# Optimization experiments

Hardware: AMD Instinct MI355X
Metric: run time of the kernel (lower is better)

## Reference

```python
import jax, jax.numpy as jnp
import numpy as np

N_NODES = 100000


def gat_conv(x, edge_index, W, att_src, att_dst, bias, concat=True, negative_slope=0.2):
    """PyG-style GATConv (eval mode, dropout off, self-loops added)."""
    N = x.shape[0]
    H, C = att_src.shape
    # add self loops (PyG default add_self_loops=True)
    ar = jnp.arange(N, dtype=edge_index.dtype)
    ei = jnp.concatenate([edge_index, jnp.stack([ar, ar])], axis=1)
    src, dst = ei[0], ei[1]

    h = (x @ W).reshape(N, H, C)                       # [N,H,C]
    a_src = (h * att_src[None]).sum(-1)                # [N,H]
    a_dst = (h * att_dst[None]).sum(-1)                # [N,H]

    e = jax.nn.leaky_relu(a_src[src] + a_dst[dst], negative_slope)  # [E,H]
    # segment softmax over destination nodes
    e_max = jax.ops.segment_max(e, dst, num_segments=N)            # [N,H]
    ex = jnp.exp(e - jax.lax.stop_gradient(e_max)[dst])
    denom = jax.ops.segment_sum(ex, dst, num_segments=N)           # [N,H]
    alpha = ex / (denom[dst] + 1e-16)                              # [E,H]

    out = jax.ops.segment_sum(alpha[:, :, None] * h[src], dst, num_segments=N)  # [N,H,C]
    out = out.reshape(N, H * C) if concat else out.mean(axis=1)
    return out + bias


def setup_inputs() -> dict:
    key = jax.random.key(0)
    ks = jax.random.split(key, 9)
    N, E, F_in, H, C = N_NODES, 3200000, 16, 4, 8
    x = jax.random.normal(ks[0], (N, F_in), dtype=jnp.float32)
    edge_index = jax.random.randint(ks[1], (2, E), 0, N, dtype=jnp.int64)
    s1 = 1.0 / np.sqrt(F_in)
    s2 = 1.0 / np.sqrt(H * C)
    return {
        "x": x,
        "edge_index": edge_index,
        "W1": jax.random.normal(ks[2], (F_in, H * C), dtype=jnp.float32) * s1,
        "att_src1": jax.random.normal(ks[3], (H, C), dtype=jnp.float32) * s2,
        "att_dst1": jax.random.normal(ks[4], (H, C), dtype=jnp.float32) * s2,
        "b1": jnp.zeros((H * C,), dtype=jnp.float32),
        "W2": jax.random.normal(ks[5], (H * C, 1), dtype=jnp.float32) * s2,
        "att_src2": jax.random.normal(ks[6], (1, 1), dtype=jnp.float32),
        "att_dst2": jax.random.normal(ks[7], (1, 1), dtype=jnp.float32),
        "b2": jnp.zeros((1,), dtype=jnp.float32),
    }


def reference(x, edge_index, W1, att_src1, att_dst1, b1, W2, att_src2, att_dst2, b2):
    h = jax.nn.elu(gat_conv(x, edge_index, W1, att_src1, att_dst1, b1, concat=True))
    return gat_conv(h, edge_index, W2, att_src2, att_dst2, b2, concat=False)
```

## Files before the change

### kernel.cpp

```cpp
#include <hip/hip_runtime.h>

#define LRELU_SLOPE 0.2f
#define BN 64
#define BSH 6
#define NC 2048
#define CAP 3840
#define TILE 16384

__device__ __forceinline__ float lrelu(float x) { return x > 0.f ? x : LRELU_SLOPE * x; }
__device__ __forceinline__ float eexp(float x)  { return __expf(fminf(x, 80.f)); }

__device__ __forceinline__ unsigned short f2bf(float f) {
    unsigned u = __float_as_uint(f);
    u += 0x7FFF + ((u >> 16) & 1);
    return (unsigned short)(u >> 16);
}
__device__ __forceinline__ float bf2f(unsigned short h) {
    return __uint_as_float((unsigned)h << 16);
}
__device__ __forceinline__ float bflo(unsigned u) {
    return __uint_as_float(u << 16);
}
__device__ __forceinline__ float bfhi(unsigned u) {
    return __uint_as_float(u & 0xFFFF0000u);
}

__global__ __launch_bounds__(256) void kA(
    const float* __restrict__ x, const float* __restrict__ W1,
    const float* __restrict__ att_src1, const float* __restrict__ att_dst1,
    unsigned short* __restrict__ h1, unsigned short* __restrict__ as1,
    float* __restrict__ ad1,
    const int* __restrict__ dst, int* __restrict__ hist, int* __restrict__ bukcnt,
    int N, int E, int nbn)
{
    __shared__ float sW[512];
    __shared__ float sAs[32], sAd[32];
    __shared__ int hl[NC];
    int tid = threadIdx.x;

    if ((int)blockIdx.x >= nbn) {
        int blk = blockIdx.x - nbn;
        for (int i = tid; i < NC; i += 256) hl[i] = 0;
        __syncthreads();
        int e0 = blk * TILE, e1 = min(e0 + TILE, E);
        for (int e = e0 + tid; e < e1; e += 256)
            atomicAdd(&hl[dst[e] >> BSH], 1);
        __syncthreads();
        for (int i = tid; i < NC; i += 256) {
            int v = hl[i];
            hist[(size_t)blk * NC + i] = v;
            if (v) atomicAdd(bukcnt + i, v);
        }
        return;
    }

    for (int i = tid; i < 512; i += 256) sW[i] = W1[i];
    if (tid < 32) { sAs[tid] = att_src1[tid]; sAd[tid] = att_dst1[tid]; }
    __syncthreads();
    int n = blockIdx.x * 256 + tid;
    if (n >= N) return;

    float xr[16];
    const float4* xp = (const float4*)(x + (size_t)n * 16);
    float4 v0 = xp[0], v1 = xp[1], v2 = xp[2], v3 = xp[3];
    xr[0]=v0.x; xr[1]=v0.y; xr[2]=v0.z;  xr[3]=v0.w;
    xr[4]=v1.x; xr[5]=v1.y; xr[6]=v1.z;  xr[7]=v1.w;
    xr[8]=v2.x; xr[9]=v2.y; xr[10]=v2.z; xr[11]=v2.w;
    xr[12]=v3.x;xr[13]=v3.y;xr[14]=v3.z; xr[15]=v3.w;

    float h[32];
#pragma unroll
    for (int j = 0; j < 32; ++j) {
        float acc = 0.f;
#pragma unroll
        for (int i = 0; i < 16; ++i) acc = fmaf(xr[i], sW[i * 32 + j], acc);
        h[j] = acc;
    }

    float asr[4], adr[4];
#pragma unroll
    for (int hh = 0; hh < 4; ++hh) {
        float as = 0.f, ad = 0.f;
#pragma unroll
        for (int c = 0; c < 8; ++c) {
            as = fmaf(h[hh * 8 + c], sAs[hh * 8 + c], as);
            ad = fmaf(h[hh * 8 + c], sAd[hh * 8 + c], ad);
        }
        asr[hh] = as; adr[hh] = ad;
    }

    ushort4* h1p = (ushort4*)(h1 + (size_t)n * 32);
#pragma unroll
    for (int j = 0; j < 32; j += 4) {
        ushort4 q;
        q.x = f2bf(h[j]); q.y = f2bf(h[j+1]); q.z = f2bf(h[j+2]); q.w = f2bf(h[j+3]);
        h1p[j >> 2] = q;
    }
    ushort4 aq;
    aq.x = f2bf(asr[0]); aq.y = f2bf(asr[1]); aq.z = f2bf(asr[2]); aq.w = f2bf(asr[3]);
    *(ushort4*)(as1 + (size_t)n * 4) = aq;
    *(float4*)(ad1 + (size_t)n * 4) = make_float4(adr[0], adr[1], adr[2], adr[3]);
}

__global__ __launch_bounds__(256) void kscan(
    const int* __restrict__ hist, int* __restrict__ histoff,
    const int* __restrict__ bukcnt, int* __restrict__ bukoff, int NBLK)
{
    __shared__ int sd[256];
    int tid = threadIdx.x;
    if ((int)blockIdx.x == NC) {
        int4 a = ((const int4*)bukcnt)[2 * tid];
        int4 c = ((const int4*)bukcnt)[2 * tid + 1];
        int tsum = a.x + a.y + a.z + a.w + c.x + c.y + c.z + c.w;
        sd[tid] = tsum; __syncthreads();
        for (int off = 1; off < 256; off <<= 1) {
            int t = (tid >= off) ? sd[tid - off] : 0; __syncthreads();
            sd[tid] += t; __syncthreads();
        }
        int excl = sd[tid] - tsum;
        int4 oa, ob;
        oa.x = excl;        oa.y = oa.x + a.x; oa.z = oa.y + a.y; oa.w = oa.z + a.z;
        ob.x = oa.w + a.w;  ob.y = ob.x + c.x; ob.z = ob.y + c.y; ob.w = ob.z + c.z;
        ((int4*)bukoff)[2 * tid] = oa;
        ((int4*)bukoff)[2 * tid + 1] = ob;
        return;
    }
    int b = blockIdx.x;
    int carry = 0;
    for (int base = 0; base < NBLK; base += 256) {
        int idx = base + tid;
        int v = (idx < NBLK) ? hist[(size_t)idx * NC + b] : 0;
        sd[tid] = v; __syncthreads();
        for (int off = 1; off < 256; off <<= 1) {
            int t = (tid >= off) ? sd[tid - off] : 0; __syncthreads();
            sd[tid] += t; __syncthreads();
        }
        int incl = sd[tid];
        int tot  = sd[255];
        if (idx < NBLK) histoff[(size_t)idx * NC + b] = carry + incl - v;
        carry += tot;
        __syncthreads();
    }
}

__global__ __launch_bounds__(512) void kpass2(
    const int* __restrict__ src, const int* __restrict__ dst,
    const int* __restrict__ hist, const int* __restrict__ histoff,
    const int* __restrict__ bukoff,
    unsigned* __restrict__ ebuk, int E)
{
    __shared__ unsigned staged[TILE];
    __shared__ int bstart[NC + 1];
    __shared__ int cur[NC];
    __shared__ int partial[512];
    int tid = threadIdx.x, blk = blockIdx.x;

    int4 c = ((const int4*)(hist + (size_t)blk * NC))[tid];
    int tsum = c.x + c.y + c.z + c.w;
    partial[tid] = tsum;
    __syncthreads();
    for (int off = 1; off < 512; off <<= 1) {
        int t = (tid >= off) ? partial[tid - off] : 0; __syncthreads();
        partial[tid] += t; __syncthreads();
    }
    int excl = partial[tid] - tsum;
    int b4 = tid * 4;
    int e0v = excl, e1v = excl + c.x, e2v = e1v + c.y, e3v = e2v + c.z;
    bstart[b4] = e0v; bstart[b4+1] = e1v; bstart[b4+2] = e2v; bstart[b4+3] = e3v;
    cur[b4] = e0v; cur[b4+1] = e1v; cur[b4+2] = e2v; cur[b4+3] = e3v;
    if (tid == 511) bstart[NC] = e3v + c.w;
    __syncthreads();

    int e0 = blk * TILE, e1 = min(e0 + TILE, E);
    for (int e = e0 + tid; e < e1; e += 512) {
        int s = src[e], d = dst[e];
        int b = d >> BSH;
        int pos = atomicAdd(&cur[b], 1);
        staged[pos] = ((unsigned)(d & (BN - 1)) << 17) | (unsigned)s;
    }
    __syncthreads();

    for (int b = tid; b < NC; b += 512) {
        int p0 = bstart[b], p1 = bstart[b + 1];
        int gb = bukoff[b] + histoff[(size_t)blk * NC + b];
        for (int p = p0; p < p1; ++p)
            ebuk[gb + (p - p0)] = staged[p];
    }
}

__global__ __launch_bounds__(256, 6) void ksort_agg1(
    unsigned* __restrict__ ebuk, const int* __restrict__ bukoff,
    const unsigned short* __restrict__ h1, const unsigned short* __restrict__ as1,
    const float* __restrict__ ad1,
    const float* __restrict__ b1, const float* __restrict__ W2,
    float* __restrict__ h2, int* __restrict__ rowptr, int N)
{
    __shared__ int sbuf[CAP];
    __shared__ int cnt[BN], exc[BN], cur[BN];
    __shared__ float sb[32], sw[32];
    int tid = threadIdx.x;
    int b = blockIdx.x;
    int n0 = b << BSH;
    int r0 = bukoff[b], r1 = bukoff[b + 1];
    int tot = r1 - r0;

    if (tid < 32) { sb[tid] = b1[tid]; sw[tid] = W2[tid]; }
    if (tid < BN) cnt[tid] = 0;
    __syncthreads();

    for (int i = tid; i < tot; i += 256)
        atomicAdd(&cnt[ebuk[r0 + i] >> 17], 1);
    __syncthreads();

    if (tid < BN) exc[tid] = cnt[tid];
    __syncthreads();
    for (int off = 1; off < BN; off <<= 1) {
        int t = 0;
        if (tid < BN && tid >= off) t = exc[tid - off];
        __syncthreads();
        if (tid < BN) exc[tid] += t;
        __syncthreads();
    }
    if (tid < BN) {
        int e = exc[tid] - cnt[tid];
        exc[tid] = e;
        cur[tid] = e;
        int n = n0 + tid;
        if (n <= N) rowptr[n] = r0 + e;
    }
    __syncthreads();

    for (int i = tid; i < tot; i += 256) {
        unsigned pk = ebuk[r0 + i];
        int dl = pk >> 17;
        int pos = atomicAdd(&cur[dl], 1);
        if (pos < CAP) sbuf[pos] = (int)(pk & 0x1FFFF);
    }
    __syncthreads();
    for (int i = tid; i < tot; i += 256)
        ebuk[r0 + i] = (unsigned)sbuf[min(i, CAP - 1)];

    int g = tid >> 2, l = tid & 3;
    {
        int dl = g;
        int n = n0 + dl;
        if (n < N) {
            float adh = ad1[(size_t)n * 4 + l];
            float ass = bf2f(as1[(size_t)n * 4 + l]);
            float wself = eexp(lrelu(ass + adh));
            float dsum = wself;
            float acc[8];
            {
                uint4 r = *(const uint4*)(h1 + (size_t)n * 32 + l * 8);
                acc[0] = wself * bflo(r.x); acc[1] = wself * bfhi(r.x);
                acc[2] = wself * bflo(r.y); acc[3] = wself * bfhi(r.y);
                acc[4] = wself * bflo(r.z); acc[5] = wself * bfhi(r.z);
                acc[6] = wself * bflo(r.w); acc[7] = wself * bfhi(r.w);
            }
            int p0 = exc[dl];
            int p1 = min(p0 + cnt[dl], CAP);
            int p = p0;
            for (; p + 4 <= p1; p += 4) {
                int sidx[4];
                float av[4];
                uint4 uv[4];
#pragma unroll
                for (int q = 0; q < 4; ++q) sidx[q] = sbuf[p + q];
#pragma unroll
                for (int q = 0; q < 4; ++q) {
                    av[q] = bf2f(as1[(size_t)sidx[q] * 4 + l]);
                    uv[q] = *(const uint4*)(h1 + (size_t)sidx[q] * 32 + l * 8);
                }
#pragma unroll
                for (int q = 0; q < 4; ++q) {
                    float w = eexp(lrelu(av[q] + adh));
                    dsum += w;
                    acc[0] = fmaf(w, bflo(uv[q].x), acc[0]);
                    acc[1] = fmaf(w, bfhi(uv[q].x), acc[1]);
                    acc[2] = fmaf(w, bflo(uv[q].y), acc[2]);
                    acc[3] = fmaf(w, bfhi(uv[q].y), acc[3]);
                    acc[4] = fmaf(w, bflo(uv[q].z), acc[4]);
                    acc[5] = fmaf(w, bfhi(uv[q].z), acc[5]);
                    acc[6] = fmaf(w, bflo(uv[q].w), acc[6]);
                    acc[7] = fmaf(w, bfhi(uv[q].w), acc[7]);
                }
            }
            for (; p < p1; ++p) {
                int s = sbuf[p];
                float ash = bf2f(as1[(size_t)s * 4 + l]);
                uint4 r = *(const uint4*)(h1 + (size_t)s * 32 + l * 8);
                float w = eexp(lrelu(ash + adh));
                dsum += w;
                acc[0] = fmaf(w, bflo(r.x), acc[0]);
                acc[1] = fmaf(w, bfhi(r.x), acc[1]);
                acc[2] = fmaf(w, bflo(r.y), acc[2]);
                acc[3] = fmaf(w, bfhi(r.y), acc[3]);
                acc[4] = fmaf(w, bflo(r.z), acc[4]);
                acc[5] = fmaf(w, bfhi(r.z), acc[5]);
                acc[6] = fmaf(w, bflo(r.w), acc[6]);
                acc[7] = fmaf(w, bfhi(r.w), acc[7]);
            }
            float inv = 1.f / (dsum + 1e-16f);
            float partial = 0.f;
#pragma unroll
            for (int ch = 0; ch < 8; ++ch) {
                float o = fmaf(acc[ch], inv, sb[l * 8 + ch]);
                o = o > 0.f ? o : __expf(o) - 1.f;
                partial = fmaf(o, sw[l * 8 + ch], partial);
            }
            partial += __shfl_xor(partial, 1);
            partial += __shfl_xor(partial, 2);
            if (l == 0) h2[n] = partial;
        }
    }
}

__global__ __launch_bounds__(256) void kagg2(
    const unsigned* __restrict__ esrc, const int* __restrict__ rowptr,
    const float* __restrict__ h2,
    const float* __restrict__ att_src2, const float* __restrict__ att_dst2,
    const float* __restrict__ b2, float* __restrict__ out, int N)
{
    int tid = threadIdx.x;
    int g = tid >> 3, l = tid & 7;
    int n = blockIdx.x * 32 + g;
    if (n >= N) return;
    float s2 = att_src2[0], d2 = att_dst2[0];
    int r0 = rowptr[n], r1 = rowptr[n + 1];
    float h2d = h2[n];
    float add = h2d * d2;
    float den = 0.f, acc = 0.f;
    if (l == 0) {
        float ws = eexp(lrelu(fmaf(h2d, s2, add)));
        den = ws; acc = ws * h2d;
    }
    for (int p = r0 + l; p < r1; p += 8) {
        int s = (int)esrc[p];
        float hs = h2[s];
        float w = eexp(lrelu(fmaf(hs, s2, add)));
        den += w;
        acc = fmaf(w, hs, acc);
    }
    den += __shfl_xor(den, 1); acc += __shfl_xor(acc, 1);
    den += __shfl_xor(den, 2); acc += __shfl_xor(acc, 2);
    den += __shfl_xor(den, 4); acc += __shfl_xor(acc, 4);
    if (l == 0) out[n] = acc / (den + 1e-16f) + b2[0];
}

extern "C" void kernel_launch(void* const* d_in, const int* in_sizes, int n_in,
                              void* d_out, int out_size, void* d_ws, size_t ws_size,
                              hipStream_t stream)
{
    const float* x        = (const float*)d_in[0];
    const int*   ei       = (const int*)d_in[1];
    const float* W1       = (const float*)d_in[2];
    const float* att_src1 = (const float*)d_in[3];
    const float* att_dst1 = (const float*)d_in[4];
    const float* b1       = (const float*)d_in[5];
    const float* W2       = (const float*)d_in[6];
    const float* att_src2 = (const float*)d_in[7];
    const float* att_dst2 = (const float*)d_in[8];
    const float* b2       = (const float*)d_in[9];

    const int N = in_sizes[0] / 16;
    const int E = in_sizes[1] / 2;
    const int* src = ei;
    const int* dst = ei + E;

    const int NBUK = (N + BN - 1) >> BSH;
    const int NBLK = (E + TILE - 1) / TILE;
    const int nb_n = (N + 255) / 256;

    unsigned short* h1  = (unsigned short*)d_ws;
    unsigned short* as1 = h1 + (size_t)N * 32;
    float* ad1   = (float*)(as1 + (size_t)N * 4);
    float* h2    = ad1 + (size_t)N * 4;
    int* rowptr  = (int*)(h2 + N);
    int* bukcnt  = rowptr + N + 64;
    int* bukoff  = bukcnt + NC;
    int* hist    = bukoff + NC;
    int* histoff = hist + (size_t)NBLK * NC;
    unsigned* ebuk = (unsigned*)(histoff + (size_t)NBLK * NC);

    hipMemsetAsync(bukcnt, 0, NC * sizeof(int), stream);

    kA<<<nb_n + NBLK, 256, 0, stream>>>(x, W1, att_src1, att_dst1,
                                        h1, as1, ad1, dst, hist, bukcnt,
                                        N, E, nb_n);
    kscan<<<NC + 1, 256, 0, stream>>>(hist, histoff, bukcnt, bukoff, NBLK);
    kpass2<<<NBLK, 512, 0, stream>>>(src, dst, hist, histoff, bukoff, ebuk, E);
    ksort_agg1<<<NBUK, 256, 0, stream>>>(ebuk, bukoff, h1, as1, ad1,
                                         b1, W2, h2, rowptr, N);
    kagg2<<<(N + 31) / 32, 256, 0, stream>>>(ebuk, rowptr, h2,
                                             att_src2, att_dst2,
                                             b2, (float*)d_out, N);
}
```

Baseline: 207.5 us.

## Store layer-1 features as FP8, batch histogram scan, widen scatter blocks

Layer-1 node features are now stored as FP8 e4m3 instead of bf16, using hardware packed converts when available. This halves the gather bytes per edge in the aggregation kernel. The column scan kernel now has each block handle 16 buckets at once with coalesced int4 row loads, replacing 2048 blocks that each did strided single-column reads. The scatter kernel moves to 1024 threads per block. FP8 lowers feature precision and may push error toward tolerance limits, and the scan assumes NBLK <= 256.

```diff
diff --git a/kernel.cpp b/kernel.cpp
--- a/kernel.cpp
+++ b/kernel.cpp
@@ -1,4 +1,5 @@
 #include <hip/hip_runtime.h>
+#include <hip/hip_fp8.h>
 
 #define LRELU_SLOPE 0.2f
 #define BN 64
@@ -18,17 +19,51 @@
 __device__ __forceinline__ float bf2f(unsigned short h) {
     return __uint_as_float((unsigned)h << 16);
 }
-__device__ __forceinline__ float bflo(unsigned u) {
-    return __uint_as_float(u << 16);
-}
-__device__ __forceinline__ float bfhi(unsigned u) {
-    return __uint_as_float(u & 0xFFFF0000u);
+
+typedef float fx2 __attribute__((ext_vector_type(2)));
+
+#if __has_builtin(__builtin_amdgcn_cvt_pk_f32_fp8) && __has_builtin(__builtin_amdgcn_cvt_pk_fp8_f32)
+#define HW_FP8 1
+#else
+#define HW_FP8 0
+#endif
+
+__device__ __forceinline__ void fp8x8_to_f32(uint2 r, float* o) {
+#if HW_FP8
+    fx2 a = __builtin_amdgcn_cvt_pk_f32_fp8((int)r.x, false);
+    fx2 b = __builtin_amdgcn_cvt_pk_f32_fp8((int)r.x, true);
+    fx2 c = __builtin_amdgcn_cvt_pk_f32_fp8((int)r.y, false);
+    fx2 d = __builtin_amdgcn_cvt_pk_f32_fp8((int)r.y, true);
+    o[0]=a.x; o[1]=a.y; o[2]=b.x; o[3]=b.y;
+    o[4]=c.x; o[5]=c.y; o[6]=d.x; o[7]=d.y;
+#else
+#pragma unroll
+    for (int i = 0; i < 8; ++i) {
+        unsigned bb = (i < 4 ? r.x : r.y) >> ((i & 3) * 8);
+        unsigned em = bb & 0x7F;
+        float f = (em >= 8) ? __uint_as_float((em << 20) + 0x3C000000u)
+                            : (float)em * 0.001953125f;
+        o[i] = (bb & 0x80) ? -f : f;
+    }
+#endif
+}
+
+__device__ __forceinline__ unsigned f32x4_to_fp8(float a, float b, float c, float d) {
+#if HW_FP8
+    int w = __builtin_amdgcn_cvt_pk_fp8_f32(a, b, 0, false);
+    w = __builtin_amdgcn_cvt_pk_fp8_f32(c, d, w, true);
+    return (unsigned)w;
+#else
+    __hip_fp8_e4m3 qa(a), qb(b), qc(c), qd(d);
+    return (unsigned)qa.__x | ((unsigned)qb.__x << 8) |
+           ((unsigned)qc.__x << 16) | ((unsigned)qd.__x << 24);
+#endif
 }
 
 __global__ __launch_bounds__(256) void kA(
     const float* __restrict__ x, const float* __restrict__ W1,
     const float* __restrict__ att_src1, const float* __restrict__ att_dst1,
-    unsigned short* __restrict__ h1, unsigned short* __restrict__ as1,
+    unsigned char* __restrict__ h1, unsigned short* __restrict__ as1,
     float* __restrict__ ad1,
     const int* __restrict__ dst, int* __restrict__ hist, int* __restrict__ bukcnt,
     int N, int E, int nbn)
@@ -89,13 +124,14 @@
         asr[hh] = as; adr[hh] = ad;
     }
 
-    ushort4* h1p = (ushort4*)(h1 + (size_t)n * 32);
-#pragma unroll
-    for (int j = 0; j < 32; j += 4) {
-        ushort4 q;
-        q.x = f2bf(h[j]); q.y = f2bf(h[j+1]); q.z = f2bf(h[j+2]); q.w = f2bf(h[j+3]);
-        h1p[j >> 2] = q;
-    }
+    unsigned q[8];
+#pragma unroll
+    for (int j = 0; j < 8; ++j)
+        q[j] = f32x4_to_fp8(h[4*j], h[4*j+1], h[4*j+2], h[4*j+3]);
+    uint4* hp = (uint4*)(h1 + (size_t)n * 32);
+    hp[0] = make_uint4(q[0], q[1], q[2], q[3]);
+    hp[1] = make_uint4(q[4], q[5], q[6], q[7]);
+
     ushort4 aq;
     aq.x = f2bf(asr[0]); aq.y = f2bf(asr[1]); aq.z = f2bf(asr[2]); aq.w = f2bf(asr[3]);
     *(ushort4*)(as1 + (size_t)n * 4) = aq;
@@ -106,9 +142,10 @@
     const int* __restrict__ hist, int* __restrict__ histoff,
     const int* __restrict__ bukcnt, int* __restrict__ bukoff, int NBLK)
 {
-    __shared__ int sd[256];
+    __shared__ int sm[256 * 17];
     int tid = threadIdx.x;
-    if ((int)blockIdx.x == NC) {
+    if ((int)blockIdx.x == NC / 16) {
+        __shared__ int sd[256];
         int4 a = ((const int4*)bukcnt)[2 * tid];
         int4 c = ((const int4*)bukcnt)[2 * tid + 1];
         int tsum = a.x + a.y + a.z + a.w + c.x + c.y + c.z + c.w;
@@ -125,25 +162,54 @@
         ((int4*)bukoff)[2 * tid + 1] = ob;
         return;
     }
-    int b = blockIdx.x;
-    int carry = 0;
-    for (int base = 0; base < NBLK; base += 256) {
-        int idx = base + tid;
-        int v = (idx < NBLK) ? hist[(size_t)idx * NC + b] : 0;
-        sd[tid] = v; __syncthreads();
-        for (int off = 1; off < 256; off <<= 1) {
-            int t = (tid >= off) ? sd[tid - off] : 0; __syncthreads();
-            sd[tid] += t; __syncthreads();
+    int c0 = blockIdx.x * 16;
+    int v[16], own[16];
+    if (tid < NBLK) {
+        const int4* rp = (const int4*)(hist + (size_t)tid * NC + c0);
+        int4 a = rp[0], b = rp[1], c = rp[2], d = rp[3];
+        v[0]=a.x; v[1]=a.y; v[2]=a.z;  v[3]=a.w;
+        v[4]=b.x; v[5]=b.y; v[6]=b.z;  v[7]=b.w;
+        v[8]=c.x; v[9]=c.y; v[10]=c.z; v[11]=c.w;
+        v[12]=d.x; v[13]=d.y; v[14]=d.z; v[15]=d.w;
+    } else {
+#pragma unroll
+        for (int i = 0; i < 16; ++i) v[i] = 0;
+    }
+#pragma unroll
+    for (int i = 0; i < 16; ++i) own[i] = v[i];
+
+    int* myrow = sm + tid * 17;
+#pragma unroll
+    for (int i = 0; i < 16; ++i) myrow[i] = v[i];
+    __syncthreads();
+    for (int off = 1; off < 256; off <<= 1) {
+        int t[16];
+        if (tid >= off) {
+            const int* nb = sm + (tid - off) * 17;
+#pragma unroll
+            for (int i = 0; i < 16; ++i) t[i] = nb[i];
+        } else {
+#pragma unroll
+            for (int i = 0; i < 16; ++i) t[i] = 0;
         }
-        int incl = sd[tid];
-        int tot  = sd[255];
-        if (idx < NBLK) histoff[(size_t)idx * NC + b] = carry + incl - v;
-        carry += tot;
-        __syncthreads();
-    }
-}
-
-__global__ __launch_bounds__(512) void kpass2(
+        __syncthreads();
+#pragma unroll
+        for (int i = 0; i < 16; ++i) { v[i] += t[i]; myrow[i] = v[i]; }
+        __syncthreads();
+    }
+    if (tid < NBLK) {
+        int4* wp = (int4*)(histoff + (size_t)tid * NC + c0);
+        int e[16];
+#pragma unroll
+        for (int i = 0; i < 16; ++i) e[i] = v[i] - own[i];
+        wp[0] = make_int4(e[0], e[1], e[2], e[3]);
+        wp[1] = make_int4(e[4], e[5], e[6], e[7]);
+        wp[2] = make_int4(e[8], e[9], e[10], e[11]);
+        wp[3] = make_int4(e[12], e[13], e[14], e[15]);
+    }
+}
+
+__global__ __launch_bounds__(1024) void kpass2(
     const int* __restrict__ src, const int* __restrict__ dst,
     const int* __restrict__ hist, const int* __restrict__ histoff,
     const int* __restrict__ bukoff,
@@ -152,27 +218,25 @@
     __shared__ unsigned staged[TILE];
     __shared__ int bstart[NC + 1];
     __shared__ int cur[NC];
-    __shared__ int partial[512];
+    __shared__ int partial[1024];
     int tid = threadIdx.x, blk = blockIdx.x;
 
-    int4 c = ((const int4*)(hist + (size_t)blk * NC))[tid];
-    int tsum = c.x + c.y + c.z + c.w;
+    int2 c2 = ((const int2*)(hist + (size_t)blk * NC))[tid];
+    int tsum = c2.x + c2.y;
     partial[tid] = tsum;
     __syncthreads();
-    for (int off = 1; off < 512; off <<= 1) {
+    for (int off = 1; off < 1024; off <<= 1) {
         int t = (tid >= off) ? partial[tid - off] : 0; __syncthreads();
         partial[tid] += t; __syncthreads();
     }
     int excl = partial[tid] - tsum;
-    int b4 = tid * 4;
-    int e0v = excl, e1v = excl + c.x, e2v = e1v + c.y, e3v = e2v + c.z;
-    bstart[b4] = e0v; bstart[b4+1] = e1v; bstart[b4+2] = e2v; bstart[b4+3] = e3v;
-    cur[b4] = e0v; cur[b4+1] = e1v; cur[b4+2] = e2v; cur[b4+3] = e3v;
-    if (tid == 511) bstart[NC] = e3v + c.w;
+    bstart[2 * tid] = excl; bstart[2 * tid + 1] = excl + c2.x;
+    cur[2 * tid] = excl;    cur[2 * tid + 1] = excl + c2.x;
+    if (tid == 1023) bstart[NC] = excl + c2.x + c2.y;
     __syncthreads();
 
     int e0 = blk * TILE, e1 = min(e0 + TILE, E);
-    for (int e = e0 + tid; e < e1; e += 512) {
+    for (int e = e0 + tid; e < e1; e += 1024) {
         int s = src[e], d = dst[e];
         int b = d >> BSH;
         int pos = atomicAdd(&cur[b], 1);
@@ -180,7 +244,7 @@
     }
     __syncthreads();
 
-    for (int b = tid; b < NC; b += 512) {
+    for (int b = tid; b < NC; b += 1024) {
         int p0 = bstart[b], p1 = bstart[b + 1];
         int gb = bukoff[b] + histoff[(size_t)blk * NC + b];
         for (int p = p0; p < p1; ++p)
@@ -190,7 +254,7 @@
 
 __global__ __launch_bounds__(256, 6) void ksort_agg1(
     unsigned* __restrict__ ebuk, const int* __restrict__ bukoff,
-    const unsigned short* __restrict__ h1, const unsigned short* __restrict__ as1,
+    const unsigned char* __restrict__ h1, const unsigned short* __restrict__ as1,
     const float* __restrict__ ad1,
     const float* __restrict__ b1, const float* __restrict__ W2,
     float* __restrict__ h2, int* __restrict__ rowptr, int N)
@@ -249,56 +313,46 @@
             float ass = bf2f(as1[(size_t)n * 4 + l]);
             float wself = eexp(lrelu(ass + adh));
             float dsum = wself;
-            float acc[8];
-            {
-                uint4 r = *(const uint4*)(h1 + (size_t)n * 32 + l * 8);
-                acc[0] = wself * bflo(r.x); acc[1] = wself * bfhi(r.x);
-                acc[2] = wself * bflo(r.y); acc[3] = wself * bfhi(r.y);
-                acc[4] = wself * bflo(r.z); acc[5] = wself * bfhi(r.z);
-                acc[6] = wself * bflo(r.w); acc[7] = wself * bfhi(r.w);
-            }
+            float acc[8], hv[8];
+            fp8x8_to_f32(*(const uint2*)(h1 + (size_t)n * 32 + l * 8), hv);
+#pragma unroll
+            for (int ch = 0; ch < 8; ++ch) acc[ch] = wself * hv[ch];
+
             int p0 = exc[dl];
             int p1 = min(p0 + cnt[dl], CAP);
             int p = p0;
             for (; p + 4 <= p1; p += 4) {
                 int sidx[4];
                 float av[4];
-                uint4 uv[4];
+                uint2 uv[4];
 #pragma unroll
                 for (int q = 0; q < 4; ++q) sidx[q] = sbuf[p + q];
 #pragma unroll
                 for (int q = 0; q < 4; ++q) {
                     av[q] = bf2f(as1[(size_t)sidx[q] * 4 + l]);
-                    uv[q] = *(const uint4*)(h1 + (size_t)sidx[q] * 32 + l * 8);
+                    uv[q] = *(const uint2*)(h1 + (size_t)sidx[q] * 32 + l * 8);
                 }
 #pragma unroll
                 for (int q = 0; q < 4; ++q) {
                     float w = eexp(lrelu(av[q] + adh));
+                    float sv[8];
+                    fp8x8_to_f32(uv[q], sv);
                     dsum += w;
-                    acc[0] = fmaf(w, bflo(uv[q].x), acc[0]);
-                    acc[1] = fmaf(w, bfhi(uv[q].x), acc[1]);
-                    acc[2] = fmaf(w, bflo(uv[q].y), acc[2]);
-                    acc[3] = fmaf(w, bfhi(uv[q].y), acc[3]);
-                    acc[4] = fmaf(w, bflo(uv[q].z), acc[4]);
-                    acc[5] = fmaf(w, bfhi(uv[q].z), acc[5]);
-                    acc[6] = fmaf(w, bflo(uv[q].w), acc[6]);
-                    acc[7] = fmaf(w, bfhi(uv[q].w), acc[7]);
+#pragma unroll
+                    for (int ch = 0; ch < 8; ++ch)
+                        acc[ch] = fmaf(w, sv[ch], acc[ch]);
                 }
             }
             for (; p < p1; ++p) {
                 int s = sbuf[p];
                 float ash = bf2f(as1[(size_t)s * 4 + l]);
-                uint4 r = *(const uint4*)(h1 + (size_t)s * 32 + l * 8);
+                float sv[8];
+                fp8x8_to_f32(*(const uint2*)(h1 + (size_t)s * 32 + l * 8), sv);
                 float w = eexp(lrelu(ash + adh));
                 dsum += w;
-                acc[0] = fmaf(w, bflo(r.x), acc[0]);
-                acc[1] = fmaf(w, bfhi(r.x), acc[1]);
-                acc[2] = fmaf(w, bflo(r.y), acc[2]);
-                acc[3] = fmaf(w, bfhi(r.y), acc[3]);
-                acc[4] = fmaf(w, bflo(r.z), acc[4]);
-                acc[5] = fmaf(w, bfhi(r.z), acc[5]);
-                acc[6] = fmaf(w, bflo(r.w), acc[6]);
-                acc[7] = fmaf(w, bfhi(r.w), acc[7]);
+#pragma unroll
+                for (int ch = 0; ch < 8; ++ch)
+                    acc[ch] = fmaf(w, sv[ch], acc[ch]);
             }
             float inv = 1.f / (dsum + 1e-16f);
             float partial = 0.f;
@@ -371,8 +425,8 @@
     const int NBLK = (E + TILE - 1) / TILE;
     const int nb_n = (N + 255) / 256;
 
-    unsigned short* h1  = (unsigned short*)d_ws;
-    unsigned short* as1 = h1 + (size_t)N * 32;
+    unsigned char* h1   = (unsigned char*)d_ws;
+    unsigned short* as1 = (unsigned short*)(h1 + (size_t)N * 32);
     float* ad1   = (float*)(as1 + (size_t)N * 4);
     float* h2    = ad1 + (size_t)N * 4;
     int* rowptr  = (int*)(h2 + N);
@@ -387,8 +441,8 @@
     kA<<<nb_n + NBLK, 256, 0, stream>>>(x, W1, att_src1, att_dst1,
                                         h1, as1, ad1, dst, hist, bukcnt,
                                         N, E, nb_n);
-    kscan<<<NC + 1, 256, 0, stream>>>(hist, histoff, bukcnt, bukoff, NBLK);
-    kpass2<<<NBLK, 512, 0, stream>>>(src, dst, hist, histoff, bukoff, ebuk, E);
+    kscan<<<NC / 16 + 1, 256, 0, stream>>>(hist, histoff, bukcnt, bukoff, NBLK);
+    kpass2<<<NBLK, 1024, 0, stream>>>(src, dst, hist, histoff, bukoff, ebuk, E);
     ksort_agg1<<<NBUK, 256, 0, stream>>>(ebuk, bukoff, h1, as1, ad1,
                                          b1, W2, h2, rowptr, N);
     kagg2<<<(N + 31) / 32, 256, 0, stream>>>(ebuk, rowptr, h2,
```

Result: faster. 196.6 us (-5.3%).
